# Optimization experiments

Hardware: AMD Instinct MI355X
Metric: run time of the kernel (lower is better)

Reference implementation:

```python
import jax, jax.numpy as jnp
import numpy as np

EPS = 1e-7
MAX_TAN_NORM = 10.0  # safe_expmap0 clamp


def logmap0(x):
    # x: [..., D] Lorentz point, x[..., 0] = time component (>= 1)
    x0 = x[..., :1]
    xs = x[..., 1:]
    d = jnp.arccosh(jnp.clip(x0, 1.0 + EPS, None))          # geodesic distance to origin
    ns = jnp.clip(jnp.linalg.norm(xs, axis=-1, keepdims=True), EPS, None)
    return jnp.concatenate([jnp.zeros_like(x0), d * xs / ns], axis=-1)


def safe_expmap0(u):
    # u: tangent at origin; time component is projected out (proju at origin)
    us = u[..., 1:]
    n = jnp.clip(jnp.linalg.norm(us, axis=-1, keepdims=True), EPS, None)
    nc = jnp.minimum(n, MAX_TAN_NORM)                        # clamp norm for stability
    usc = us * (nc / n)
    return jnp.concatenate([jnp.cosh(nc), jnp.sinh(nc) * usc / nc], axis=-1)


def projx(x):
    # re-project onto the hyperboloid: x0 = sqrt(1 + ||xs||^2)
    xs = x[..., 1:]
    x0 = jnp.sqrt(1.0 + jnp.sum(xs * xs, axis=-1, keepdims=True))
    return jnp.concatenate([x0, xs], axis=-1)


def lorentz_linear(x_hyp, W, b):
    t = logmap0(x_hyp)
    y = t @ W.T + b
    return projx(safe_expmap0(y))


def setup_inputs() -> dict:
    key = jax.random.key(0)
    ks = jax.random.split(key, 8)
    N, D_IN, D_HID, D_OUT = 8192, 1024, 4096, 1024
    s = 0.02
    x_sp = jax.random.normal(ks[0], (N, D_IN), dtype=jnp.float32)
    x_hyp = projx(x_sp)  # valid Lorentz point (time comp overwritten)
    W1 = jax.random.normal(ks[1], (D_HID, D_IN), dtype=jnp.float32) * s
    b1 = jnp.zeros((D_HID,), dtype=jnp.float32)
    W2 = jax.random.normal(ks[2], (D_HID, D_HID), dtype=jnp.float32) * s
    b2 = jnp.zeros((D_HID,), dtype=jnp.float32)
    W3 = jax.random.normal(ks[3], (D_OUT, D_HID), dtype=jnp.float32) * s
    b3 = jnp.zeros((D_OUT,), dtype=jnp.float32)
    return {"x_hyp": x_hyp, "W1": W1, "b1": b1, "W2": W2, "b2": b2, "W3": W3, "b3": b3}


def reference(x_hyp, W1, b1, W2, b2, W3, b3):
    # layers[:-1] with inter-layer logmap0 -> (dropout=identity in eval) -> expmap0 -> projx
    h = lorentz_linear(x_hyp, W1, b1)
    h = projx(safe_expmap0(logmap0(h)))
    h = lorentz_linear(h, W2, b2)
    h = projx(safe_expmap0(logmap0(h)))
    return lorentz_linear(h, W3, b3)
```

## Files before the change

kernel.cpp:

```cpp
#include <hip/hip_runtime.h>
#include <stdint.h>

#define EPSF 1e-7f
#define MAXTAN 10.0f

typedef __bf16 bf16x8 __attribute__((ext_vector_type(8)));
typedef float floatx4 __attribute__((ext_vector_type(4)));
typedef __attribute__((address_space(3))) void lds_void_t;
typedef __attribute__((address_space(1))) void gbl_void_t;

__device__ __forceinline__ unsigned short f2bf(float x) {
  union { float f; uint32_t u; } v; v.f = x;
  uint32_t u = v.u;
  u += 0x7fffu + ((u >> 16) & 1u);
  return (unsigned short)(u >> 16);
}
__device__ __forceinline__ float bf2f(unsigned short h) {
  union { uint32_t u; float f; } v; v.u = ((uint32_t)h) << 16;
  return v.f;
}

__device__ __forceinline__ int sniff_mode(const unsigned short* x) {
  int sane = 0;
  for (int i = 0; i < 128; ++i) {
    unsigned short h = x[i];
    int e = (h >> 7) & 0xFF;
    if ((h & 0x7FFF) == 0 || (e >= 96 && e <= 140)) ++sane;
  }
  return (sane >= 120) ? 1 : 0;
}

__global__ void k_init(const unsigned short* __restrict__ x, int* __restrict__ modeg,
                       const void* __restrict__ b1, const void* __restrict__ b2,
                       const void* __restrict__ b3, float* __restrict__ o1,
                       float* __restrict__ o2, float* __restrict__ o3) {
  __shared__ int mds;
  if (threadIdx.x == 0) {
    int m = sniff_mode(x);
    mds = m;
    if (blockIdx.x == 0) *modeg = m;
  }
  __syncthreads();
  int m = mds;
  int i = blockIdx.x * 256 + threadIdx.x;
  if (i < 4096) o1[i] = m ? bf2f(((const unsigned short*)b1)[i]) : ((const float*)b1)[i];
  if (i < 4096) o2[i] = m ? bf2f(((const unsigned short*)b2)[i]) : ((const float*)b2)[i];
  if (i < 1024) o3[i] = m ? bf2f(((const unsigned short*)b3)[i]) : ((const float*)b3)[i];
}

__global__ void k_prep(const void* __restrict__ xv, unsigned short* __restrict__ xb,
                       float* __restrict__ sc0, float* __restrict__ x0c,
                       const int* __restrict__ mode) {
  const int row = blockIdx.x;
  const int tid = threadIdx.x;
  float4 v;
  if (*mode) {
    ushort4 u = ((const ushort4*)((const unsigned short*)xv + (size_t)row * 1024))[tid];
    v.x = bf2f(u.x); v.y = bf2f(u.y); v.z = bf2f(u.z); v.w = bf2f(u.w);
  } else {
    v = ((const float4*)((const float*)xv + (size_t)row * 1024))[tid];
  }
  ushort4 o;
  o.x = f2bf(v.x); o.y = f2bf(v.y); o.z = f2bf(v.z); o.w = f2bf(v.w);
  ((ushort4*)(xb + (size_t)row * 1024))[tid] = o;

  float s = v.x * v.x + v.y * v.y + v.z * v.z + v.w * v.w;
  if (tid == 0) s -= v.x * v.x;
  for (int off = 32; off; off >>= 1) s += __shfl_down(s, off, 64);
  __shared__ float red[4];
  if ((tid & 63) == 0) red[tid >> 6] = s;
  __syncthreads();
  if (tid == 0) {
    s = red[0] + red[1] + red[2] + red[3];
    float ns = fmaxf(sqrtf(s), EPSF);
    float d = acoshf(fmaxf(v.x, 1.0f + EPSF));
    sc0[row] = d / ns;
    x0c[row] = bf2f(o.x);
  }
}

template<int K8>
__global__ void k_cvtw(const void* __restrict__ in, unsigned short* __restrict__ out,
                       const int* __restrict__ mode, int n8, float* __restrict__ c0) {
  int i = blockIdx.x * 256 + threadIdx.x;
  if (i >= n8) return;
  if (*mode) {
    uint4 g = ((const uint4*)in)[i];
    ((uint4*)out)[i] = g;
    if (i % K8 == 0) c0[i / K8] = bf2f((unsigned short)(g.x & 0xFFFFu));
  } else {
    float4 a = ((const float4*)in)[2 * i];
    float4 b = ((const float4*)in)[2 * i + 1];
    ushort4 oa, ob;
    oa.x = f2bf(a.x); oa.y = f2bf(a.y); oa.z = f2bf(a.z); oa.w = f2bf(a.w);
    ob.x = f2bf(b.x); ob.y = f2bf(b.y); ob.z = f2bf(b.z); ob.w = f2bf(b.w);
    ((ushort4*)out)[2 * i] = oa;
    ((ushort4*)out)[2 * i + 1] = ob;
    if (i % K8 == 0) c0[i / K8] = bf2f(oa.x);
  }
}

template<int NBLK>
__global__ void k_sc(const float* __restrict__ part, const unsigned short* __restrict__ y,
                     int stride, float* __restrict__ sc, float* __restrict__ c0,
                     float* __restrict__ ssout, int nrows) {
  int i = blockIdx.x * 256 + threadIdx.x;
  if (i >= nrows) return;
  float s = 0.f;
#pragma unroll
  for (int j = 0; j < NBLK; ++j) s += part[(size_t)i * NBLK + j];
  float n = fmaxf(sqrtf(fmaxf(s, 0.f)), EPSF);
  sc[i] = fminf(n, MAXTAN) / n;
  c0[i] = bf2f(y[(size_t)i * stride]);
  if (ssout) ssout[i] = s;
}

__global__ void k_final(const unsigned short* __restrict__ y, const float* __restrict__ ss,
                        void* __restrict__ outv, const int* __restrict__ mode) {
  const int row = blockIdx.x;
  const int tid = threadIdx.x;
  float n = fmaxf(sqrtf(fmaxf(ss[row], 0.f)), EPSF);
  float nc = fminf(n, MAXTAN);
  float a = sinhf(nc) / n;
  ushort4 u = ((const ushort4*)(y + (size_t)row * 1024))[tid];
  float4 o;
  o.x = bf2f(u.x) * a; o.y = bf2f(u.y) * a;
  o.z = bf2f(u.z) * a; o.w = bf2f(u.w) * a;
  if (tid == 0) o.x = coshf(nc);
  if (*mode) {
    ushort4 o16;
    o16.x = f2bf(o.x); o16.y = f2bf(o.y); o16.z = f2bf(o.z); o16.w = f2bf(o.w);
    ((ushort4*)outv)[(size_t)row * 256 + tid] = o16;
  } else {
    ((float4*)outv)[(size_t)row * 256 + tid] = o;
  }
}

template<int N, int K, int NBLK, int GX>
__global__ __launch_bounds__(256, 4) void k_gemm_bt(
    const unsigned short* __restrict__ A,
    const unsigned short* __restrict__ B,
    const float* __restrict__ bias,
    const float* __restrict__ sc,
    const float* __restrict__ c0f,
    const float* __restrict__ wc0,
    unsigned short* __restrict__ Cb,
    float* __restrict__ part)
{
  __shared__ __align__(16) unsigned short As[128 * 32];
  __shared__ __align__(16) unsigned short Bs[128 * 32];

  const int tid  = threadIdx.x;
  const int wave = tid >> 6;
  const int lane = tid & 63;
  const int quad = lane >> 4;
  const int m16  = lane & 15;

  const int j = blockIdx.x & 7;
  const int k = blockIdx.x >> 3;
  int bxi, byi;
  if (GX == 32) {
    bxi = 16 * (j & 1) + (k & 15);
    byi = 16 * (j >> 1) + (k >> 4);
  } else {
    bxi = k & 7;
    byi = 8 * j + (k >> 3);
  }
  const int bm = byi * 128;
  const int bn = bxi * 128;

  const int srow = lane >> 2;
  const int scol = (((lane & 3) ^ ((srow >> 1) & 3)) << 3);

  const int wm = (wave >> 1) << 6;
  const int wn = (wave & 1) << 6;

  const int rsw = ((quad ^ ((m16 >> 1) & 3)) << 3);

  const int c0i = wave * 2;
  const unsigned short* ga0 = A + (size_t)(bm + c0i * 16 + srow) * K + scol;
  const unsigned short* ga1 = ga0 + (size_t)16 * K;
  const unsigned short* gb0 = B + (size_t)(bn + c0i * 16 + srow) * K + scol;
  const unsigned short* gb1 = gb0 + (size_t)16 * K;

  floatx4 acc[4][4];
#pragma unroll
  for (int i = 0; i < 4; ++i)
#pragma unroll
    for (int jj = 0; jj < 4; ++jj)
#pragma unroll
      for (int r = 0; r < 4; ++r) acc[i][jj][r] = 0.0f;

  for (int k0 = 0; k0 < K; k0 += 32) {
    __builtin_amdgcn_global_load_lds((gbl_void_t*)(void*)ga0,
                                     (lds_void_t*)(As + c0i * 512), 16, 0, 0);
    __builtin_amdgcn_global_load_lds((gbl_void_t*)(void*)ga1,
                                     (lds_void_t*)(As + c0i * 512 + 512), 16, 0, 0);
    __builtin_amdgcn_global_load_lds((gbl_void_t*)(void*)gb0,
                                     (lds_void_t*)(Bs + c0i * 512), 16, 0, 0);
    __builtin_amdgcn_global_load_lds((gbl_void_t*)(void*)gb1,
                                     (lds_void_t*)(Bs + c0i * 512 + 512), 16, 0, 0);
    ga0 += 32; ga1 += 32; gb0 += 32; gb1 += 32;
    __syncthreads();

    bf16x8 af[4], bfg[4];
#pragma unroll
    for (int t = 0; t < 4; ++t) {
      af[t]  = *(const bf16x8*)(As + (wm + t * 16 + m16) * 32 + rsw);
      bfg[t] = *(const bf16x8*)(Bs + (wn + t * 16 + m16) * 32 + rsw);
    }
#pragma unroll
    for (int mt = 0; mt < 4; ++mt)
#pragma unroll
      for (int nt = 0; nt < 4; ++nt)
        acc[mt][nt] = __builtin_amdgcn_mfma_f32_16x16x32_bf16(af[mt], bfg[nt], acc[mt][nt], 0, 0, 0);
    __syncthreads();
  }

#pragma unroll
  for (int mt = 0; mt < 4; ++mt) {
#pragma unroll
    for (int r = 0; r < 4; ++r) {
      const int gm = bm + wm + mt * 16 + quad * 4 + r;
      const float scv = sc[gm];
      const float c0v = c0f[gm];
      float sq = 0.f;
#pragma unroll
      for (int nt = 0; nt < 4; ++nt) {
        const int gn = bn + wn + nt * 16 + m16;
        float v = scv * (acc[mt][nt][r] - c0v * wc0[gn]) + bias[gn];
        Cb[(size_t)gm * N + gn] = f2bf(v);
        sq += (gn == 0) ? 0.f : v * v;
      }
      sq += __shfl_xor(sq, 1, 64);
      sq += __shfl_xor(sq, 2, 64);
      sq += __shfl_xor(sq, 4, 64);
      sq += __shfl_xor(sq, 8, 64);
      if (m16 == 0) part[(size_t)gm * NBLK + 2 * bxi + (wave & 1)] = sq;
    }
  }
}

template<int N, int K>
__global__ __launch_bounds__(512, 2) void k_gemm256(
    const unsigned short* __restrict__ A,
    const unsigned short* __restrict__ B,
    const float* __restrict__ bias,
    const float* __restrict__ sc,
    const float* __restrict__ c0f,
    const float* __restrict__ wc0,
    unsigned short* __restrict__ Cb,
    float* __restrict__ part)
{
  static_assert(K % 64 == 0 && K / 32 >= 4, "need even NT >= 4");
  constexpr int NT = K / 32;
  __shared__ __align__(16) unsigned short S[4][2][8192];

  const int tid  = threadIdx.x;
  const int wave = tid >> 6;
  const int lane = tid & 63;
  const int quad = lane >> 4;
  const int m16  = lane & 15;
  const int wr   = wave >> 2;
  const int wc   = wave & 3;

  const int j = blockIdx.x & 7;
  const int k = blockIdx.x >> 3;
  const int bxi = 8 * (j & 1) + (k & 7);
  const int byi = 8 * (j >> 1) + (k >> 3);
  const int bm = byi * 256;
  const int bn = bxi * 256;

  const int gsw8 = (((tid & 3) ^ ((tid >> 3) & 3)) << 3);
  const unsigned short* gA = A + (size_t)(bm + (tid >> 2)) * K + gsw8;
  const unsigned short* gB = B + (size_t)(bn + (tid >> 2)) * K + gsw8;
  const int ld0 = wave * 512;
  const int ld1 = 4096 + wave * 512;

  const int rsw8 = ((quad ^ ((m16 >> 1) & 3)) << 3);
  const int aoff = (wr * 128 + m16) * 32 + rsw8;
  const int boff = (wc * 64  + m16) * 32 + rsw8;

  floatx4 acc[8][4];
#pragma unroll
  for (int i = 0; i < 8; ++i)
#pragma unroll
    for (int jj = 0; jj < 4; ++jj)
#pragma unroll
      for (int r = 0; r < 4; ++r) acc[i][jj][r] = 0.0f;

#define GLL(SRC, DST) __builtin_amdgcn_global_load_lds((gbl_void_t*)(void*)(SRC), (lds_void_t*)(DST), 16, 0, 0)

#pragma unroll
  for (int tt = 0; tt < 3; ++tt) {
    const unsigned short* pa = gA + tt * 32;
    const unsigned short* pb = gB + tt * 32;
    GLL(pa,                   &S[tt][0][ld0]);
    GLL(pa + (size_t)128 * K, &S[tt][0][ld1]);
    GLL(pb,                   &S[tt][1][ld0]);
    GLL(pb + (size_t)128 * K, &S[tt][1][ld1]);
  }
  asm volatile("s_waitcnt vmcnt(4)" ::: "memory");
  __builtin_amdgcn_s_barrier();

  bf16x8 aX[4], bX[4], aY[4], bY[4];
#pragma unroll
  for (int f = 0; f < 4; ++f) aX[f] = *(const bf16x8*)(&S[0][0][0] + aoff + f * 512);
#pragma unroll
  for (int n = 0; n < 4; ++n) bX[n] = *(const bf16x8*)(&S[0][1][0] + boff + n * 512);

#define ITER(T, AC, BC, AN, BN)                                                        \
  {                                                                                    \
    const int slot_ = (T) & 3;                                                         \
    const int s3_   = ((T) + 3) & 3;                                                   \
    const int kt_   = ((T) + 3 < NT ? (T) + 3 : NT - 1) * 32;                          \
    GLL(gA + kt_,                   &S[s3_][0][ld0]);                                  \
    GLL(gA + kt_ + (size_t)128 * K, &S[s3_][0][ld1]);                                  \
    GLL(gB + kt_,                   &S[s3_][1][ld0]);                                  \
    GLL(gB + kt_ + (size_t)128 * K, &S[s3_][1][ld1]);                                  \
    bf16x8 a2_[4];                                                                     \
    _Pragma("unroll")                                                                  \
    for (int f = 0; f < 4; ++f)                                                        \
      a2_[f] = *(const bf16x8*)(&S[slot_][0][0] + aoff + 2048 + f * 512);              \
    __builtin_amdgcn_s_setprio(1);                                                     \
    _Pragma("unroll")                                                                  \
    for (int f = 0; f < 4; ++f)                                                        \
      _Pragma("unroll")                                                                \
      for (int n = 0; n < 4; ++n)                                                      \
        acc[f][n] = __builtin_amdgcn_mfma_f32_16x16x32_bf16(AC[f], BC[n], acc[f][n], 0, 0, 0); \
    __builtin_amdgcn_s_setprio(0);                                                     \
    const int sn_ = ((T) + 1 < NT ? (T) + 1 : NT - 1) & 3;                             \
    _Pragma("unroll")                                                                  \
    for (int f = 0; f < 4; ++f)                                                        \
      AN[f] = *(const bf16x8*)(&S[sn_][0][0] + aoff + f * 512);                        \
    _Pragma("unroll")                                                                  \
    for (int n = 0; n < 4; ++n)                                                        \
      BN[n] = *(const bf16x8*)(&S[sn_][1][0] + boff + n * 512);                        \
    __builtin_amdgcn_s_setprio(1);                                                     \
    _Pragma("unroll")                                                                  \
    for (int f = 0; f < 4; ++f)                                                        \
      _Pragma("unroll")                                                                \
      for (int n = 0; n < 4; ++n)                                                      \
        acc[f + 4][n] = __builtin_amdgcn_mfma_f32_16x16x32_bf16(a2_[f], BC[n], acc[f + 4][n], 0, 0, 0); \
    __builtin_amdgcn_s_setprio(0);                                                     \
    asm volatile("s_waitcnt vmcnt(4)" ::: "memory");                                   \
    __builtin_amdgcn_s_barrier();                                                      \
  }

  for (int t = 0; t < NT; t += 2) {
    ITER(t,     aX, bX, aY, bY)
    ITER(t + 1, aY, bY, aX, bX)
  }
#undef ITER
#undef GLL

  asm volatile("s_waitcnt vmcnt(0)" ::: "memory");

  const int wm = wr * 128;
  const int wn = wc * 64;
#pragma unroll
  for (int mt = 0; mt < 8; ++mt) {
#pragma unroll
    for (int r = 0; r < 4; ++r) {
      const int gm = bm + wm + mt * 16 + quad * 4 + r;
      const float scv = sc[gm];
      const float c0v = c0f[gm];
      float sq = 0.f;
#pragma unroll
      for (int nt = 0; nt < 4; ++nt) {
        const int gn = bn + wn + nt * 16 + m16;
        float v = scv * (acc[mt][nt][r] - c0v * wc0[gn]) + bias[gn];
        Cb[(size_t)gm * N + gn] = f2bf(v);
        sq += (gn == 0) ? 0.f : v * v;
      }
      sq += __shfl_xor(sq, 1, 64);
      sq += __shfl_xor(sq, 2, 64);
      sq += __shfl_xor(sq, 4, 64);
      sq += __shfl_xor(sq, 8, 64);
      if (m16 == 0) part[(size_t)gm * 64 + bxi * 4 + wc] = sq;
    }
  }
}

extern "C" void kernel_launch(void* const* d_in, const int* in_sizes, int n_in,
                              void* d_out, int out_size, void* d_ws, size_t ws_size,
                              hipStream_t stream) {
  const void* x  = d_in[0];
  const void* W1 = d_in[1];
  const void* b1 = d_in[2];
  const void* W2 = d_in[3];
  const void* b2 = d_in[4];
  const void* W3 = d_in[5];
  const void* b3 = d_in[6];

  const int NR = 8192, DIN = 1024, DH = 4096, DOUT = 1024;

  char* ws = (char*)d_ws;
  size_t off = 0;
  int* mode = (int*)(ws + off);                        off += 256;
  unsigned short* W1b = (unsigned short*)(ws + off);   off += (size_t)DH * DIN * 2;
  unsigned short* W2b = (unsigned short*)(ws + off);   off += (size_t)DH * DH * 2;
  unsigned short* W3b = (unsigned short*)(ws + off);   off += (size_t)DOUT * DH * 2;
  unsigned short* xb  = (unsigned short*)(ws + off);   off += (size_t)NR * DIN * 2;
  unsigned short* y1  = (unsigned short*)(ws + off);   off += (size_t)NR * DH * 2;
  unsigned short* y2  = (unsigned short*)(ws + off);   off += (size_t)NR * DH * 2;
  unsigned short* y3  = (unsigned short*)(ws + off);   off += (size_t)NR * DOUT * 2;
  float* part1 = (float*)(ws + off);                   off += (size_t)NR * 64 * 4;
  float* part2 = (float*)(ws + off);                   off += (size_t)NR * 64 * 4;
  float* part3 = (float*)(ws + off);                   off += (size_t)NR * 16 * 4;
  float* sc0  = (float*)(ws + off);                    off += (size_t)NR * 4;
  float* x0c  = (float*)(ws + off);                    off += (size_t)NR * 4;
  float* sc1  = (float*)(ws + off);                    off += (size_t)NR * 4;
  float* c01  = (float*)(ws + off);                    off += (size_t)NR * 4;
  float* sc2  = (float*)(ws + off);                    off += (size_t)NR * 4;
  float* c02  = (float*)(ws + off);                    off += (size_t)NR * 4;
  float* ss3  = (float*)(ws + off);                    off += (size_t)NR * 4;
  float* w1c0 = (float*)(ws + off);                    off += (size_t)DH * 4;
  float* w2c0 = (float*)(ws + off);                    off += (size_t)DH * 4;
  float* w3c0 = (float*)(ws + off);                    off += (size_t)DOUT * 4;
  float* b1f  = (float*)(ws + off);                    off += (size_t)DH * 4;
  float* b2f  = (float*)(ws + off);                    off += (size_t)DH * 4;
  float* b3f  = (float*)(ws + off);                    off += (size_t)DOUT * 4;

  k_init<<<16, 256, 0, stream>>>((const unsigned short*)x, mode, b1, b2, b3, b1f, b2f, b3f);

  k_cvtw<128><<<(DH * DIN / 8 + 255) / 256, 256, 0, stream>>>(W1, W1b, mode, DH * DIN / 8, w1c0);
  k_cvtw<512><<<(DH * DH  / 8 + 255) / 256, 256, 0, stream>>>(W2, W2b, mode, DH * DH / 8, w2c0);
  k_cvtw<512><<<(DOUT * DH / 8 + 255) / 256, 256, 0, stream>>>(W3, W3b, mode, DOUT * DH / 8, w3c0);

  k_prep<<<NR, 256, 0, stream>>>(x, xb, sc0, x0c, mode);

  k_gemm256<4096, 1024><<<512, 512, 0, stream>>>(
      xb, W1b, b1f, sc0, x0c, w1c0, y1, part1);
  k_sc<64><<<(NR + 255) / 256, 256, 0, stream>>>(part1, y1, DH, sc1, c01, nullptr, NR);

  k_gemm256<4096, 4096><<<512, 512, 0, stream>>>(
      y1, W2b, b2f, sc1, c01, w2c0, y2, part2);
  k_sc<64><<<(NR + 255) / 256, 256, 0, stream>>>(part2, y2, DH, sc2, c02, nullptr, NR);

  k_gemm_bt<1024, 4096, 16, 8><<<512, 256, 0, stream>>>(
      y2, W3b, b3f, sc2, c02, w3c0, y3, part3);
  k_sc<16><<<(NR + 255) / 256, 256, 0, stream>>>(part3, y3, DOUT, sc0, x0c, ss3, NR);

  k_final<<<NR, 256, 0, stream>>>(y3, ss3, d_out, mode);
}
```

Measured before the change: 608.7 us.

## Unroll GEMM K-loop by four with constant LDS offsets and peeled epilogue

Restructures the 256x256 bf16 GEMM main loop so the 4-slot LDS ring is unrolled by four. Every LDS read and global_load_lds destination then uses compile-time byte offsets from a few base pointers, and the global pointers advance once per four steps. The last K tiles are peeled so no redundant clamped loads are issued and the waits drain properly. It also loads all eight A fragments at once instead of holding A double-buffered in registers, aiming to cut address arithmetic and register pressure at the cost of larger code and a stricter K-divisibility requirement.

Result: faster. 594.1 us (-2.4%).

```diff
diff --git a/kernel.cpp b/kernel.cpp
--- a/kernel.cpp
+++ b/kernel.cpp
@@ -252,7 +252,7 @@
     unsigned short* __restrict__ Cb,
     float* __restrict__ part)
 {
-  static_assert(K % 64 == 0 && K / 32 >= 4, "need even NT >= 4");
+  static_assert(K % 128 == 0 && K / 32 >= 8, "need NT multiple of 4, >= 8");
   constexpr int NT = K / 32;
   __shared__ __align__(16) unsigned short S[4][2][8192];
 
@@ -272,14 +272,20 @@
   const int bn = bxi * 256;
 
   const int gsw8 = (((tid & 3) ^ ((tid >> 3) & 3)) << 3);
-  const unsigned short* gA = A + (size_t)(bm + (tid >> 2)) * K + gsw8;
-  const unsigned short* gB = B + (size_t)(bn + (tid >> 2)) * K + gsw8;
-  const int ld0 = wave * 512;
-  const int ld1 = 4096 + wave * 512;
+  const unsigned short* gAp = A + (size_t)(bm + (tid >> 2)) * K + gsw8;
+  const unsigned short* gAq = gAp + (size_t)128 * K;
+  const unsigned short* gBp = B + (size_t)(bn + (tid >> 2)) * K + gsw8;
+  const unsigned short* gBq = gBp + (size_t)128 * K;
+  const int ldw = wave * 1024;
 
   const int rsw8 = ((quad ^ ((m16 >> 1) & 3)) << 3);
-  const int aoff = (wr * 128 + m16) * 32 + rsw8;
-  const int boff = (wc * 64  + m16) * 32 + rsw8;
+  const int aoffB = ((wr * 128 + m16) * 32 + rsw8) * 2;
+  const int boffB = ((wc * 64  + m16) * 32 + rsw8) * 2;
+  const char* Sb  = (const char*)&S[0][0][0];
+  const char* pA  = Sb + aoffB;
+  const char* pA2 = pA + 65536;
+  const char* pB  = Sb + 16384 + boffB;
+  const char* pB2 = pB + 65536;
 
   floatx4 acc[8][4];
 #pragma unroll
@@ -290,71 +296,149 @@
       for (int r = 0; r < 4; ++r) acc[i][jj][r] = 0.0f;
 
 #define GLL(SRC, DST) __builtin_amdgcn_global_load_lds((gbl_void_t*)(void*)(SRC), (lds_void_t*)(DST), 16, 0, 0)
-
-#pragma unroll
-  for (int tt = 0; tt < 3; ++tt) {
-    const unsigned short* pa = gA + tt * 32;
-    const unsigned short* pb = gB + tt * 32;
-    GLL(pa,                   &S[tt][0][ld0]);
-    GLL(pa + (size_t)128 * K, &S[tt][0][ld1]);
-    GLL(pb,                   &S[tt][1][ld0]);
-    GLL(pb + (size_t)128 * K, &S[tt][1][ld1]);
-  }
+#define ARD(S_, M_) (*(const bf16x8*)(((S_) < 2 ? pA : pA2) + ((S_) * 32768 + (M_) * 1024 - ((S_) < 2 ? 0 : 65536))))
+#define BRD(S_, N_) (*(const bf16x8*)(((S_) < 2 ? pB : pB2) + ((S_) * 32768 + (N_) * 1024 - ((S_) < 2 ? 0 : 65536))))
+#define STG(T_, OFF) { \
+    GLL(gAp + (OFF), (char*)Sb + (T_) * 32768 +         ldw); \
+    GLL(gAq + (OFF), (char*)Sb + (T_) * 32768 +  8192 + ldw); \
+    GLL(gBp + (OFF), (char*)Sb + (T_) * 32768 + 16384 + ldw); \
+    GLL(gBq + (OFF), (char*)Sb + (T_) * 32768 + 24576 + ldw); }
+
+  STG(0, 0) STG(1, 32) STG(2, 64)
   asm volatile("s_waitcnt vmcnt(4)" ::: "memory");
   __builtin_amdgcn_s_barrier();
 
-  bf16x8 aX[4], bX[4], aY[4], bY[4];
-#pragma unroll
-  for (int f = 0; f < 4; ++f) aX[f] = *(const bf16x8*)(&S[0][0][0] + aoff + f * 512);
-#pragma unroll
-  for (int n = 0; n < 4; ++n) bX[n] = *(const bf16x8*)(&S[0][1][0] + boff + n * 512);
-
-#define ITER(T, AC, BC, AN, BN)                                                        \
+  bf16x8 bX[4], bY[4];
+#pragma unroll
+  for (int n = 0; n < 4; ++n) bX[n] = BRD(0, n);
+
+#define MBODY(BI, BC, BN)                                                              \
   {                                                                                    \
-    const int slot_ = (T) & 3;                                                         \
-    const int s3_   = ((T) + 3) & 3;                                                   \
-    const int kt_   = ((T) + 3 < NT ? (T) + 3 : NT - 1) * 32;                          \
-    GLL(gA + kt_,                   &S[s3_][0][ld0]);                                  \
-    GLL(gA + kt_ + (size_t)128 * K, &S[s3_][0][ld1]);                                  \
-    GLL(gB + kt_,                   &S[s3_][1][ld0]);                                  \
-    GLL(gB + kt_ + (size_t)128 * K, &S[s3_][1][ld1]);                                  \
-    bf16x8 a2_[4];                                                                     \
-    _Pragma("unroll")                                                                  \
-    for (int f = 0; f < 4; ++f)                                                        \
-      a2_[f] = *(const bf16x8*)(&S[slot_][0][0] + aoff + 2048 + f * 512);              \
+    STG((BI + 3) & 3, (BI + 3) * 32)                                                   \
+    bf16x8 a_[8];                                                                      \
+    _Pragma("unroll")                                                                  \
+    for (int m = 0; m < 8; ++m) a_[m] = ARD(BI, m);                                    \
     __builtin_amdgcn_s_setprio(1);                                                     \
     _Pragma("unroll")                                                                  \
     for (int f = 0; f < 4; ++f)                                                        \
       _Pragma("unroll")                                                                \
       for (int n = 0; n < 4; ++n)                                                      \
-        acc[f][n] = __builtin_amdgcn_mfma_f32_16x16x32_bf16(AC[f], BC[n], acc[f][n], 0, 0, 0); \
+        acc[f][n] = __builtin_amdgcn_mfma_f32_16x16x32_bf16(a_[f], BC[n], acc[f][n], 0, 0, 0); \
     __builtin_amdgcn_s_setprio(0);                                                     \
-    const int sn_ = ((T) + 1 < NT ? (T) + 1 : NT - 1) & 3;                             \
-    _Pragma("unroll")                                                                  \
-    for (int f = 0; f < 4; ++f)                                                        \
-      AN[f] = *(const bf16x8*)(&S[sn_][0][0] + aoff + f * 512);                        \
-    _Pragma("unroll")                                                                  \
-    for (int n = 0; n < 4; ++n)                                                        \
-      BN[n] = *(const bf16x8*)(&S[sn_][1][0] + boff + n * 512);                        \
+    _Pragma("unroll")                                                                  \
+    for (int n = 0; n < 4; ++n) BN[n] = BRD((BI + 1) & 3, n);                          \
     __builtin_amdgcn_s_setprio(1);                                                     \
     _Pragma("unroll")                                                                  \
     for (int f = 0; f < 4; ++f)                                                        \
       _Pragma("unroll")                                                                \
       for (int n = 0; n < 4; ++n)                                                      \
-        acc[f + 4][n] = __builtin_amdgcn_mfma_f32_16x16x32_bf16(a2_[f], BC[n], acc[f + 4][n], 0, 0, 0); \
+        acc[f + 4][n] = __builtin_amdgcn_mfma_f32_16x16x32_bf16(a_[f + 4], BC[n], acc[f + 4][n], 0, 0, 0); \
     __builtin_amdgcn_s_setprio(0);                                                     \
     asm volatile("s_waitcnt vmcnt(4)" ::: "memory");                                   \
     __builtin_amdgcn_s_barrier();                                                      \
   }
 
-  for (int t = 0; t < NT; t += 2) {
-    ITER(t,     aX, bX, aY, bY)
-    ITER(t + 1, aY, bY, aX, bX)
-  }
-#undef ITER
+#define TBODY(BI, BC)                                                                  \
+  {                                                                                    \
+    bf16x8 a_[8];                                                                      \
+    _Pragma("unroll")                                                                  \
+    for (int m = 0; m < 8; ++m) a_[m] = ARD(BI, m);                                    \
+    __builtin_amdgcn_s_setprio(1);                                                     \
+    _Pragma("unroll")                                                                  \
+    for (int f = 0; f < 4; ++f)                                                        \
+      _Pragma("unroll")                                                                \
+      for (int n = 0; n < 4; ++n)                                                      \
+        acc[f][n] = __builtin_amdgcn_mfma_f32_16x16x32_bf16(a_[f], BC[n], acc[f][n], 0, 0, 0); \
+    _Pragma("unroll")                                                                  \
+    for (int f = 0; f < 4; ++f)                                                        \
+      _Pragma("unroll")                                                                \
+      for (int n = 0; n < 4; ++n)                                                      \
+        acc[f + 4][n] = __builtin_amdgcn_mfma_f32_16x16x32_bf16(a_[f + 4], BC[n], acc[f + 4][n], 0, 0, 0); \
+    __builtin_amdgcn_s_setprio(0);                                                     \
+  }
+
+  for (int t = 0; t < NT - 4; t += 4) {
+    MBODY(0, bX, bY)
+    MBODY(1, bY, bX)
+    MBODY(2, bX, bY)
+    MBODY(3, bY, bX)
+    gAp += 128; gAq += 128; gBp += 128; gBq += 128;
+  }
+
+  STG(3, 96)
+  {
+    bf16x8 a_[8];
+#pragma unroll
+    for (int m = 0; m < 8; ++m) a_[m] = ARD(0, m);
+    __builtin_amdgcn_s_setprio(1);
+#pragma unroll
+    for (int f = 0; f < 4; ++f)
+#pragma unroll
+      for (int n = 0; n < 4; ++n)
+        acc[f][n] = __builtin_amdgcn_mfma_f32_16x16x32_bf16(a_[f], bX[n], acc[f][n], 0, 0, 0);
+    __builtin_amdgcn_s_setprio(0);
+#pragma unroll
+    for (int n = 0; n < 4; ++n) bY[n] = BRD(1, n);
+    __builtin_amdgcn_s_setprio(1);
+#pragma unroll
+    for (int f = 0; f < 4; ++f)
+#pragma unroll
+      for (int n = 0; n < 4; ++n)
+        acc[f + 4][n] = __builtin_amdgcn_mfma_f32_16x16x32_bf16(a_[f + 4], bX[n], acc[f + 4][n], 0, 0, 0);
+    __builtin_amdgcn_s_setprio(0);
+  }
+  asm volatile("s_waitcnt vmcnt(0)" ::: "memory");
+  __builtin_amdgcn_s_barrier();
+  {
+    bf16x8 a_[8];
+#pragma unroll
+    for (int m = 0; m < 8; ++m) a_[m] = ARD(1, m);
+    __builtin_amdgcn_s_setprio(1);
+#pragma unroll
+    for (int f = 0; f < 4; ++f)
+#pragma unroll
+      for (int n = 0; n < 4; ++n)
+        acc[f][n] = __builtin_amdgcn_mfma_f32_16x16x32_bf16(a_[f], bY[n], acc[f][n], 0, 0, 0);
+    __builtin_amdgcn_s_setprio(0);
+#pragma unroll
+    for (int n = 0; n < 4; ++n) bX[n] = BRD(2, n);
+    __builtin_amdgcn_s_setprio(1);
+#pragma unroll
+    for (int f = 0; f < 4; ++f)
+#pragma unroll
+      for (int n = 0; n < 4; ++n)
+        acc[f + 4][n] = __builtin_amdgcn_mfma_f32_16x16x32_bf16(a_[f + 4], bY[n], acc[f + 4][n], 0, 0, 0);
+    __builtin_amdgcn_s_setprio(0);
+  }
+  {
+    bf16x8 a_[8];
+#pragma unroll
+    for (int m = 0; m < 8; ++m) a_[m] = ARD(2, m);
+    __builtin_amdgcn_s_setprio(1);
+#pragma unroll
+    for (int f = 0; f < 4; ++f)
+#pragma unroll
+      for (int n = 0; n < 4; ++n)
+        acc[f][n] = __builtin_amdgcn_mfma_f32_16x16x32_bf16(a_[f], bX[n], acc[f][n], 0, 0, 0);
+    __builtin_amdgcn_s_setprio(0);
+#pragma unroll
+    for (int n = 0; n < 4; ++n) bY[n] = BRD(3, n);
+    __builtin_amdgcn_s_setprio(1);
+#pragma unroll
+    for (int f = 0; f < 4; ++f)
+#pragma unroll
+      for (int n = 0; n < 4; ++n)
+        acc[f + 4][n] = __builtin_amdgcn_mfma_f32_16x16x32_bf16(a_[f + 4], bX[n], acc[f + 4][n], 0, 0, 0);
+    __builtin_amdgcn_s_setprio(0);
+  }
+  TBODY(3, bY)
+
+#undef TBODY
+#undef MBODY
+#undef STG
+#undef BRD
+#undef ARD
 #undef GLL
-
-  asm volatile("s_waitcnt vmcnt(0)" ::: "memory");
 
   const int wm = wr * 128;
   const int wn = wc * 64;
```

## Replace 256x256 GEMM tile with 128x256 four-wave kernel and 3-stage pipeline

Applied to the files above, without the earlier changes.

Replaces the 512-thread, 256x256-tile GEMM used for the first two layers with a 256-thread, 128x256-tile kernel. Each wave now computes all 128 rows against its own 64 columns, and the kernel uses a 3-slot LDS ring buffer with loads issued two k-steps ahead instead of a 4-slot ring with register double-buffering. The aim is smaller LDS use and a 1024-block grid for better occupancy and load balance. In exchange it adds more B-tile traffic per output and drops the overlap of LDS fragment reads with MFMA work.

Result: no change. 610.5 us (+0.3%).

```diff
diff --git a/kernel.cpp b/kernel.cpp
--- a/kernel.cpp
+++ b/kernel.cpp
@@ -242,7 +242,7 @@
 }
 
 template<int N, int K>
-__global__ __launch_bounds__(512, 2) void k_gemm256(
+__global__ __launch_bounds__(256, 2) void k_g128(
     const unsigned short* __restrict__ A,
     const unsigned short* __restrict__ B,
     const float* __restrict__ bias,
@@ -252,34 +252,38 @@
     unsigned short* __restrict__ Cb,
     float* __restrict__ part)
 {
-  static_assert(K % 64 == 0 && K / 32 >= 4, "need even NT >= 4");
   constexpr int NT = K / 32;
-  __shared__ __align__(16) unsigned short S[4][2][8192];
+  static_assert(NT >= 5 && (NT - 2) % 3 == 0, "NT must be 2 mod 3, >=5");
+  constexpr int NBX = N / 256;
+  static_assert(NBX == 16, "grid swizzle assumes N==4096");
+  __shared__ __align__(16) unsigned short S[3][12288];
 
   const int tid  = threadIdx.x;
-  const int wave = tid >> 6;
+  const int wc   = tid >> 6;
   const int lane = tid & 63;
   const int quad = lane >> 4;
   const int m16  = lane & 15;
-  const int wr   = wave >> 2;
-  const int wc   = wave & 3;
-
-  const int j = blockIdx.x & 7;
-  const int k = blockIdx.x >> 3;
-  const int bxi = 8 * (j & 1) + (k & 7);
-  const int byi = 8 * (j >> 1) + (k >> 3);
-  const int bm = byi * 256;
+
+  const int j  = blockIdx.x & 7;
+  const int kk = blockIdx.x >> 3;
+  const int bxi = 8 * (j & 1) + (kk & 7);
+  const int byi = 16 * (j >> 1) + (kk >> 3);
+  const int bm = byi * 128;
   const int bn = bxi * 256;
 
   const int gsw8 = (((tid & 3) ^ ((tid >> 3) & 3)) << 3);
-  const unsigned short* gA = A + (size_t)(bm + (tid >> 2)) * K + gsw8;
-  const unsigned short* gB = B + (size_t)(bn + (tid >> 2)) * K + gsw8;
-  const int ld0 = wave * 512;
-  const int ld1 = 4096 + wave * 512;
+  const int srow = tid >> 2;
+  const unsigned short* pA0 = A + (size_t)(bm + srow) * K + gsw8;
+  const unsigned short* pA1 = pA0 + (size_t)64 * K;
+  const unsigned short* pB0 = B + (size_t)(bn + srow) * K + gsw8;
+  const unsigned short* pB1 = pB0 + (size_t)64 * K;
+  const unsigned short* pB2 = pB0 + (size_t)128 * K;
+  const unsigned short* pB3 = pB0 + (size_t)192 * K;
+  char* LDw = (char*)&S[0][0] + wc * 1024;
 
   const int rsw8 = ((quad ^ ((m16 >> 1) & 3)) << 3);
-  const int aoff = (wr * 128 + m16) * 32 + rsw8;
-  const int boff = (wc * 64  + m16) * 32 + rsw8;
+  const char* Ab = (const char*)&S[0][0] + m16 * 64 + rsw8 * 2;
+  const char* Bb = (const char*)&S[0][0] + 8192 + (wc * 64 + m16) * 64 + rsw8 * 2;
 
   floatx4 acc[8][4];
 #pragma unroll
@@ -290,85 +294,85 @@
       for (int r = 0; r < 4; ++r) acc[i][jj][r] = 0.0f;
 
 #define GLL(SRC, DST) __builtin_amdgcn_global_load_lds((gbl_void_t*)(void*)(SRC), (lds_void_t*)(DST), 16, 0, 0)
-
-#pragma unroll
-  for (int tt = 0; tt < 3; ++tt) {
-    const unsigned short* pa = gA + tt * 32;
-    const unsigned short* pb = gB + tt * 32;
-    GLL(pa,                   &S[tt][0][ld0]);
-    GLL(pa + (size_t)128 * K, &S[tt][0][ld1]);
-    GLL(pb,                   &S[tt][1][ld0]);
-    GLL(pb + (size_t)128 * K, &S[tt][1][ld1]);
-  }
-  asm volatile("s_waitcnt vmcnt(4)" ::: "memory");
+#define STG(SL, CO) { \
+    GLL(pA0 + (CO), LDw + (SL) * 24576 +     0); \
+    GLL(pA1 + (CO), LDw + (SL) * 24576 +  4096); \
+    GLL(pB0 + (CO), LDw + (SL) * 24576 +  8192); \
+    GLL(pB1 + (CO), LDw + (SL) * 24576 + 12288); \
+    GLL(pB2 + (CO), LDw + (SL) * 24576 + 16384); \
+    GLL(pB3 + (CO), LDw + (SL) * 24576 + 20480); }
+#define ARD(SL, M_) (*(const bf16x8*)(Ab + (SL) * 24576 + (M_) * 1024))
+#define BRD(SL, N_) (*(const bf16x8*)(Bb + (SL) * 24576 + (N_) * 1024))
+
+  STG(0, 0) STG(1, 32)
+  pA0 += 64; pA1 += 64; pB0 += 64; pB1 += 64; pB2 += 64; pB3 += 64;
+  asm volatile("s_waitcnt vmcnt(6)" ::: "memory");
   __builtin_amdgcn_s_barrier();
 
-  bf16x8 aX[4], bX[4], aY[4], bY[4];
-#pragma unroll
-  for (int f = 0; f < 4; ++f) aX[f] = *(const bf16x8*)(&S[0][0][0] + aoff + f * 512);
-#pragma unroll
-  for (int n = 0; n < 4; ++n) bX[n] = *(const bf16x8*)(&S[0][1][0] + boff + n * 512);
-
-#define ITER(T, AC, BC, AN, BN)                                                        \
+#define BODY(SC, SS, CO)                                                               \
   {                                                                                    \
-    const int slot_ = (T) & 3;                                                         \
-    const int s3_   = ((T) + 3) & 3;                                                   \
-    const int kt_   = ((T) + 3 < NT ? (T) + 3 : NT - 1) * 32;                          \
-    GLL(gA + kt_,                   &S[s3_][0][ld0]);                                  \
-    GLL(gA + kt_ + (size_t)128 * K, &S[s3_][0][ld1]);                                  \
-    GLL(gB + kt_,                   &S[s3_][1][ld0]);                                  \
-    GLL(gB + kt_ + (size_t)128 * K, &S[s3_][1][ld1]);                                  \
-    bf16x8 a2_[4];                                                                     \
-    _Pragma("unroll")                                                                  \
-    for (int f = 0; f < 4; ++f)                                                        \
-      a2_[f] = *(const bf16x8*)(&S[slot_][0][0] + aoff + 2048 + f * 512);              \
+    STG(SS, CO)                                                                        \
+    bf16x8 a_[8], b_[4];                                                               \
+    _Pragma("unroll")                                                                  \
+    for (int m = 0; m < 8; ++m) a_[m] = ARD(SC, m);                                    \
+    _Pragma("unroll")                                                                  \
+    for (int n = 0; n < 4; ++n) b_[n] = BRD(SC, n);                                    \
     __builtin_amdgcn_s_setprio(1);                                                     \
     _Pragma("unroll")                                                                  \
-    for (int f = 0; f < 4; ++f)                                                        \
+    for (int f = 0; f < 8; ++f)                                                        \
       _Pragma("unroll")                                                                \
       for (int n = 0; n < 4; ++n)                                                      \
-        acc[f][n] = __builtin_amdgcn_mfma_f32_16x16x32_bf16(AC[f], BC[n], acc[f][n], 0, 0, 0); \
+        acc[f][n] = __builtin_amdgcn_mfma_f32_16x16x32_bf16(a_[f], b_[n], acc[f][n], 0, 0, 0); \
     __builtin_amdgcn_s_setprio(0);                                                     \
-    const int sn_ = ((T) + 1 < NT ? (T) + 1 : NT - 1) & 3;                             \
-    _Pragma("unroll")                                                                  \
-    for (int f = 0; f < 4; ++f)                                                        \
-      AN[f] = *(const bf16x8*)(&S[sn_][0][0] + aoff + f * 512);                        \
-    _Pragma("unroll")                                                                  \
-    for (int n = 0; n < 4; ++n)                                                        \
-      BN[n] = *(const bf16x8*)(&S[sn_][1][0] + boff + n * 512);                        \
+    asm volatile("s_waitcnt vmcnt(6)" ::: "memory");                                   \
+    __builtin_amdgcn_s_barrier();                                                      \
+  }
+#define TBODY(SC)                                                                      \
+  {                                                                                    \
+    bf16x8 a_[8], b_[4];                                                               \
+    _Pragma("unroll")                                                                  \
+    for (int m = 0; m < 8; ++m) a_[m] = ARD(SC, m);                                    \
+    _Pragma("unroll")                                                                  \
+    for (int n = 0; n < 4; ++n) b_[n] = BRD(SC, n);                                    \
     __builtin_amdgcn_s_setprio(1);                                                     \
     _Pragma("unroll")                                                                  \
-    for (int f = 0; f < 4; ++f)                                                        \
+    for (int f = 0; f < 8; ++f)                                                        \
       _Pragma("unroll")                                                                \
       for (int n = 0; n < 4; ++n)                                                      \
-        acc[f + 4][n] = __builtin_amdgcn_mfma_f32_16x16x32_bf16(a2_[f], BC[n], acc[f + 4][n], 0, 0, 0); \
+        acc[f][n] = __builtin_amdgcn_mfma_f32_16x16x32_bf16(a_[f], b_[n], acc[f][n], 0, 0, 0); \
     __builtin_amdgcn_s_setprio(0);                                                     \
-    asm volatile("s_waitcnt vmcnt(4)" ::: "memory");                                   \
-    __builtin_amdgcn_s_barrier();                                                      \
-  }
-
-  for (int t = 0; t < NT; t += 2) {
-    ITER(t,     aX, bX, aY, bY)
-    ITER(t + 1, aY, bY, aX, bX)
-  }
-#undef ITER
+  }
+
+  for (int g = 0; g < (NT - 2) / 3; ++g) {
+    BODY(0, 2, 0)
+    BODY(1, 0, 32)
+    BODY(2, 1, 64)
+    pA0 += 96; pA1 += 96; pB0 += 96; pB1 += 96; pB2 += 96; pB3 += 96;
+  }
+
+  TBODY(0)
+  asm volatile("s_waitcnt vmcnt(0)" ::: "memory");
+  __builtin_amdgcn_s_barrier();
+  TBODY(1)
+
+#undef TBODY
+#undef BODY
+#undef ARD
+#undef BRD
+#undef STG
 #undef GLL
 
-  asm volatile("s_waitcnt vmcnt(0)" ::: "memory");
-
-  const int wm = wr * 128;
-  const int wn = wc * 64;
 #pragma unroll
   for (int mt = 0; mt < 8; ++mt) {
 #pragma unroll
     for (int r = 0; r < 4; ++r) {
-      const int gm = bm + wm + mt * 16 + quad * 4 + r;
+      const int gm = bm + mt * 16 + quad * 4 + r;
       const float scv = sc[gm];
       const float c0v = c0f[gm];
       float sq = 0.f;
 #pragma unroll
       for (int nt = 0; nt < 4; ++nt) {
-        const int gn = bn + wn + nt * 16 + m16;
+        const int gn = bn + wc * 64 + nt * 16 + m16;
         float v = scv * (acc[mt][nt][r] - c0v * wc0[gn]) + bias[gn];
         Cb[(size_t)gm * N + gn] = f2bf(v);
         sq += (gn == 0) ? 0.f : v * v;
@@ -377,7 +381,7 @@
       sq += __shfl_xor(sq, 2, 64);
       sq += __shfl_xor(sq, 4, 64);
       sq += __shfl_xor(sq, 8, 64);
-      if (m16 == 0) part[(size_t)gm * 64 + bxi * 4 + wc] = sq;
+      if (m16 == 0) part[(size_t)gm * (4 * NBX) + bxi * 4 + wc] = sq;
     }
   }
 }
@@ -430,11 +434,11 @@
 
   k_prep<<<NR, 256, 0, stream>>>(x, xb, sc0, x0c, mode);
 
-  k_gemm256<4096, 1024><<<512, 512, 0, stream>>>(
+  k_g128<4096, 1024><<<1024, 256, 0, stream>>>(
       xb, W1b, b1f, sc0, x0c, w1c0, y1, part1);
   k_sc<64><<<(NR + 255) / 256, 256, 0, stream>>>(part1, y1, DH, sc1, c01, nullptr, NR);
 
-  k_gemm256<4096, 4096><<<512, 512, 0, stream>>>(
+  k_g128<4096, 4096><<<1024, 256, 0, stream>>>(
       y1, W2b, b2f, sc1, c01, w2c0, y2, part2);
   k_sc<64><<<(NR + 255) / 256, 256, 0, stream>>>(part2, y2, DH, sc2, c02, nullptr, NR);
 
```
